# Kernel optimization log

Measured on AMD Instinct MI355X. Metric: run time of the kernel, lower is better.

Reference implementation:

```python
import jax, jax.numpy as jnp
import numpy as np

B, T, N, K, C = 4, 12, 2000, 8, 32
AGG_N = 4  # mean, max, min, std
EPS = 1e-5


def sparsify(a, k):
    # keep top-k entries per row, zero the rest (torch.topk + torch.where)
    thr = jax.lax.top_k(a, k)[0][..., -1:]
    return jnp.where(a < thr, jnp.zeros_like(a), a)


def aggregate(I, adj):
    # I: (b,t,n,f), adj: (b,n,n) row-sparsified with K nonzeros per row
    deg = jnp.sum(adj, axis=-1)[:, None, :, None]              # (b,1,n,1)
    mean = jnp.einsum('bnm,btmf->btnf', adj, I) / deg
    meansq = jnp.einsum('bnm,btmf->btnf', adj, I * I) / deg
    std = jnp.sqrt(jax.nn.relu(meansq - mean * mean) + EPS)
    vals, idx = jax.lax.top_k(adj, K)                          # (b,n,K)
    nb = jax.vmap(lambda Ib, ib: Ib[:, ib])(I, idx)            # (b,t,n,K,f)
    valid = (vals > 0)[:, None, :, :, None]
    mx = jnp.max(jnp.where(valid, nb, -jnp.inf), axis=3)
    mn = jnp.min(jnp.where(valid, nb, jnp.inf), axis=3)
    return jnp.concatenate([mean, mx, mn, std], axis=3)


def stower(x, adj, Theta, bias, masking, use_scalers):
    # x: (b,c,t,n) -> out: (b,o,t,n)
    I = jnp.transpose(x, (0, 2, 3, 1))                          # (b,t,n,c)
    m = aggregate(I, adj)
    if masking:
        m = jnp.where(jnp.isnan(m), 6.0, m)
        m = jnp.where(jnp.isinf(m), 0.0, m)
        m = jnp.minimum(m, 6.0)
    if use_scalers:
        deg = jnp.sum((adj > 0).astype(m.dtype), axis=-1)       # (b,n)
        s = jnp.log1p(deg)[:, None, :, None]
        m = jnp.concatenate([m, m * s, m / s], axis=3)
    out = jnp.einsum('btji,io->btjo', m, Theta) + bias
    return jnp.transpose(out, (0, 3, 1, 2))


def tcn(x, W, b):
    # tcn_layer2 with act='linear': tanh(conv1x1(x) + x)
    return jnp.tanh(jnp.einsum('oc,bctn->botn', W, x) + b[None, :, None, None] + x)


def setup_inputs():
    key = jax.random.key(0)
    ks = jax.random.split(key, 14)
    stdv = 1.0 / np.sqrt(C)
    u = lambda k, shape: jax.random.uniform(k, shape, jnp.float32, -stdv, stdv)
    return {
        'X': jax.random.normal(ks[0], (B, T, N, 1), jnp.float32),
        'adj': jax.random.uniform(ks[1], (N, N), jnp.float32),
        'adj_mask': jax.random.uniform(ks[2], (N, N), jnp.float32),
        'Theta0': u(ks[3], (AGG_N * 1, C)),   # len(agg)*len(['identity'])*in_variables
        'bias0': u(ks[4], (C,)),
        'Wt0': u(ks[5], (C, C)),
        'bt0': u(ks[6], (C,)),
        'Theta1': u(ks[7], (AGG_N * 3 * C, C)),  # len(agg)*len(scalers)*channels
        'bias1': u(ks[8], (C,)),
        'Wt1': u(ks[9], (C, C)),
        'bt1': u(ks[10], (C,)),
        'Wout': u(ks[11], (1, C)),
        'bout': u(ks[12], (1,)),
        'batch_seen': 0,
        'epoch': 0,
        'train': 0,
    }


def reference(X, adj, adj_mask, Theta0, bias0, Wt0, bt0, Theta1, bias1, Wt1, bt1, Wout, bout, batch_seen, epoch, train):
    x0 = X[:, None, :, :, 0]                                   # (b,1,t,n)
    adj_s = sparsify(jnp.broadcast_to(adj, (B, N, N)), K)
    adjm_s = sparsify(jnp.broadcast_to(adj_mask, (B, N, N)), K)
    h = stower(x0, adjm_s, Theta0, bias0, True, False)         # s_layer0 (masking, identity scaler)
    h = tcn(h, Wt0, bt0)                                       # t_layer0
    h = jax.nn.relu(stower(h, adj_s, Theta1, bias1, False, True))
    h = jax.nn.relu(tcn(h, Wt1, bt1))
    y = jnp.einsum('oc,bctn->botn', Wout, h) + bout[None, :, None, None]
    return y.reshape(B, T, N)
```

## Files before the change

kernel.cpp:

```cpp
#include <hip/hip_runtime.h>
#include <hip/hip_bf16.h>
#include <math.h>

#define BB 4
#define TT 12
#define NN 2000
#define KK 8
#define CC 32
#define EPSF 1e-5f
#define LISTCAP 16
#define NSITES (BB * TT * NN)

typedef unsigned short u16;
typedef __bf16 bf16x8 __attribute__((ext_vector_type(8)));
typedef float  f32x4  __attribute__((ext_vector_type(4)));

__device__ __forceinline__ u16 f2bf(float x) {
    union { __hip_bfloat16 h; u16 u; } c;
    c.h = __float2bfloat16(x);
    return c.u;
}
__device__ __forceinline__ float bf2f(u16 u) {
    return __uint_as_float(((unsigned)u) << 16);
}
__device__ __forceinline__ float mask6(float v) {
    if (isnan(v)) v = 6.0f;
    if (isinf(v)) v = 0.0f;
    return fminf(v, 6.0f);
}

__global__ __launch_bounds__(256)
void topk_prep(const float* __restrict__ adj, const float* __restrict__ adjm,
               int* __restrict__ t_idx, float* __restrict__ t_val,
               int* __restrict__ t_cnt, float* __restrict__ t_deg,
               float* __restrict__ t_ideg, float2* __restrict__ t_sc)
{
    __shared__ float sTop[4][8];
    __shared__ float sDeg[4];
    __shared__ int   sCp[4];
    __shared__ int   sStrictIdx[8];
    __shared__ float sStrictVal[8];
    __shared__ int   sTieIdx[16];
    __shared__ int   nStrict, nTie;
    __shared__ float sThr;

    const int tid  = threadIdx.x;
    const int lane = tid & 63;
    const int wid  = tid >> 6;

    const int grow = blockIdx.x;
    const int mat = (grow >= NN) ? 1 : 0;
    const int row = grow - mat * NN;
    const float* src = (mat == 0 ? adjm : adj) + (size_t)row * NN;
    const float4* src4 = (const float4*)src;

    if (tid == 0) { nStrict = 0; nTie = 0; }

    const float4 v0 = src4[tid];
    const float4 v1 = (tid < 244) ? src4[256 + tid]
                                  : make_float4(-1.f, -1.f, -1.f, -1.f);
    const float vv[8] = {v0.x, v0.y, v0.z, v0.w, v1.x, v1.y, v1.z, v1.w};

    float a[8];
    #pragma unroll
    for (int j = 0; j < 8; ++j) a[j] = vv[j];
    #define CE(i, j) { float _mx = fmaxf(a[i], a[j]); float _mn = fminf(a[i], a[j]); a[i] = _mx; a[j] = _mn; }
    CE(0,1) CE(2,3) CE(4,5) CE(6,7)
    CE(0,2) CE(1,3) CE(4,6) CE(5,7)
    CE(1,2) CE(5,6)
    CE(0,4) CE(1,5) CE(2,6) CE(3,7)
    CE(2,4) CE(3,5)
    CE(1,2) CE(3,4) CE(5,6)
    #undef CE

    float key[8];
    #pragma unroll
    for (int j = 0; j < 8; ++j) key[j] = a[j];
    #pragma unroll
    for (int d = 1; d < 64; d <<= 1) {
        float ok[8], c[8];
        #pragma unroll
        for (int j = 0; j < 8; ++j) ok[j] = __shfl_xor(key[j], d, 64);
        #pragma unroll
        for (int j = 0; j < 8; ++j) c[j] = fmaxf(key[j], ok[7 - j]);
        #pragma unroll
        for (int st = 4; st >= 1; st >>= 1) {
            #pragma unroll
            for (int j = 0; j < 8; ++j) {
                if ((j & st) == 0 && (j | st) < 8) {
                    float hi = fmaxf(c[j], c[j | st]);
                    float lo = fminf(c[j], c[j | st]);
                    c[j] = hi; c[j | st] = lo;
                }
            }
        }
        #pragma unroll
        for (int j = 0; j < 8; ++j) key[j] = c[j];
    }
    if (lane == 0) {
        #pragma unroll
        for (int j = 0; j < 8; ++j) sTop[wid][j] = key[j];
    }
    __syncthreads();

    if (tid == 0) {
        int p0 = 0, p1 = 0, p2 = 0, p3 = 0;
        float t = -1.f;
        for (int r = 0; r < 8; ++r) {
            const float c0 = (p0 < 8) ? sTop[0][p0] : -2.f;
            const float c1 = (p1 < 8) ? sTop[1][p1] : -2.f;
            const float c2 = (p2 < 8) ? sTop[2][p2] : -2.f;
            const float c3 = (p3 < 8) ? sTop[3][p3] : -2.f;
            float bv = c0; int best = 0;
            if (c1 > bv) { bv = c1; best = 1; }
            if (c2 > bv) { bv = c2; best = 2; }
            if (c3 > bv) { bv = c3; best = 3; }
            if (best == 0) ++p0; else if (best == 1) ++p1;
            else if (best == 2) ++p2; else ++p3;
            t = bv;
        }
        sThr = t;
    }
    __syncthreads();
    const float thr = sThr;

    float degp = 0.f; int cp = 0;
    #pragma unroll
    for (int s = 0; s < 8; ++s) {
        const float v = vv[s];
        const int e = (s < 4) ? (tid * 4 + s) : ((256 + tid) * 4 + (s - 4));
        const bool ge = (v >= thr);
        degp += ge ? v : 0.f;
        cp   += (ge && v > 0.f) ? 1 : 0;
        if (v > thr) {
            int p = atomicAdd(&nStrict, 1);
            if (p < 8) { sStrictIdx[p] = e; sStrictVal[p] = v; }
        } else if (v == thr) {
            int p = atomicAdd(&nTie, 1);
            if (p < 16) sTieIdx[p] = e;
        }
    }
    #pragma unroll
    for (int off = 32; off >= 1; off >>= 1) {
        degp += __shfl_xor(degp, off, 64);
        cp   += __shfl_xor(cp, off, 64);
    }
    if (lane == 0) { sDeg[wid] = degp; sCp[wid] = cp; }
    __syncthreads();

    if (tid == 0) {
        const float deg = sDeg[0] + sDeg[1] + sDeg[2] + sDeg[3];
        const int cnt_pos = sCp[0] + sCp[1] + sCp[2] + sCp[3];
        int m = nStrict; if (m > 8) m = 8;
        int nt = nTie;   if (nt > 16) nt = 16;
        for (int i = 1; i < nt; ++i) {
            int v = sTieIdx[i]; int j = i - 1;
            while (j >= 0 && sTieIdx[j] > v) { sTieIdx[j + 1] = sTieIdx[j]; --j; }
            sTieIdx[j + 1] = v;
        }
        const size_t ob = (size_t)grow * LISTCAP;
        for (int j = 0; j < m; ++j) {
            t_idx[ob + j] = sStrictIdx[j];
            t_val[ob + j] = sStrictVal[j];
        }
        const int need = 8 - m;
        for (int j = 0; j < need; ++j) {
            t_idx[ob + m + j] = sTieIdx[j];
            t_val[ob + m + j] = thr;
        }
        int extra = nt - need;
        if (extra > 8) extra = 8; if (extra < 0) extra = 0;
        for (int j = 0; j < extra; ++j) {
            t_idx[ob + 8 + j] = sTieIdx[need + j];
            t_val[ob + 8 + j] = thr;
        }
        t_cnt[grow]  = 8 + extra;
        t_deg[grow]  = deg;
        t_ideg[grow] = 1.0f / deg;
        const float s1 = log1pf((float)cnt_pos);
        t_sc[grow]   = make_float2(s1, 1.0f / s1);
    }
}

__global__ __launch_bounds__(256)
void stower0_tcn0(const float* __restrict__ X,
                  const int* __restrict__ t_idx, const float* __restrict__ t_val,
                  const int* __restrict__ t_cnt, const float* __restrict__ t_deg,
                  const float* __restrict__ Theta0, const float* __restrict__ bias0,
                  const float* __restrict__ Wt0, const float* __restrict__ bt0,
                  const float* __restrict__ Theta1, const float* __restrict__ Wt1,
                  u16* __restrict__ thHi, u16* __restrict__ thLo,
                  u16* __restrict__ wtHi, u16* __restrict__ wtLo,
                  float* __restrict__ I1)
{
    const int tid = threadIdx.x;
    if (blockIdx.x >= NSITES / 256) {
        const int pb = blockIdx.x - NSITES / 256;
        if (pb < 12) {
            const int base = pb * 1024;
            #pragma unroll
            for (int t = 0; t < 4; ++t) {
                const int i = base + t * 256 + tid;
                const int r = i >> 5, o = i & 31;
                const int jm = r >> 7, k = r & 127;
                const int tile = jm * 2 + (o >> 4), n = o & 15;
                const float v = Theta1[i];
                const u16 hi = f2bf(v);
                const int idx = (tile * 16 + n) * 128 + (((k >> 3) ^ n) << 3) + (k & 7);
                thHi[idx] = hi;
                thLo[idx] = f2bf(v - bf2f(hi));
            }
        } else {
            #pragma unroll
            for (int t = 0; t < 4; ++t) {
                const int i = t * 256 + tid;
                const float v = Wt1[i];
                const u16 hi = f2bf(v);
                wtHi[i] = hi;
                wtLo[i] = f2bf(v - bf2f(hi));
            }
        }
        return;
    }

    const int site = blockIdx.x * 256 + tid;
    const int n  = site % NN;
    const int bt = site / NN;
    const float* xrow = X + (size_t)bt * NN;

    const size_t base = (size_t)n * LISTCAP;
    const int cnt   = t_cnt[n];
    const float deg = t_deg[n];
    float wsum = 0.f, wsq = 0.f, mx = -INFINITY, mn = INFINITY;
    for (int j = 0; j < cnt; ++j) {
        int   id = t_idx[base + j];
        float w  = t_val[base + j];
        float xv = xrow[id];
        wsum = fmaf(w, xv, wsum);
        wsq  = fmaf(w * xv, xv, wsq);
        if (j < KK && w > 0.f) { mx = fmaxf(mx, xv); mn = fminf(mn, xv); }
    }
    float mean = wsum / deg;
    float var  = wsq / deg - mean * mean;
    float sd   = sqrtf(fmaxf(var, 0.f) + EPSF);
    float m0 = mask6(mean), m1 = mask6(mx), m2 = mask6(mn), m3 = mask6(sd);

    float h0[CC];
    #pragma unroll
    for (int c = 0; c < CC; ++c) {
        float v = bias0[c];
        v = fmaf(m0, Theta0[0 * CC + c], v);
        v = fmaf(m1, Theta0[1 * CC + c], v);
        v = fmaf(m2, Theta0[2 * CC + c], v);
        v = fmaf(m3, Theta0[3 * CC + c], v);
        h0[c] = v;
    }
    float* op = I1 + (size_t)site * CC;
    #pragma unroll
    for (int c = 0; c < CC; ++c) {
        float acc = bt0[c] + h0[c];
        #pragma unroll
        for (int k = 0; k < CC; ++k) acc = fmaf(Wt0[c * CC + k], h0[k], acc);
        op[c] = tanhf(acc);
    }
}

__global__ __launch_bounds__(256)
void stower1_agg(const float* __restrict__ I1,
                 const int* __restrict__ t_idx, const float* __restrict__ t_val,
                 const int* __restrict__ t_cnt, const float* __restrict__ t_ideg,
                 u16* __restrict__ mHi, u16* __restrict__ mLo)
{
    const int tid  = threadIdx.x;
    const int site = blockIdx.x * 8 + (tid >> 5);
    const int f    = tid & 31;
    const int n  = site % NN;
    const int bt = site / NN;
    const size_t rbase = (size_t)(NN + n) * LISTCAP;
    const int cnt    = t_cnt[NN + n];
    const float ideg = t_ideg[NN + n];
    const float* Ibt = I1 + (size_t)bt * NN * CC;

    const int4   i0 = *(const int4*)&t_idx[rbase];
    const int4   i1 = *(const int4*)&t_idx[rbase + 4];
    const float4 w0 = *(const float4*)&t_val[rbase];
    const float4 w1 = *(const float4*)&t_val[rbase + 4];

    const float x0 = Ibt[(size_t)i0.x * CC + f];
    const float x1 = Ibt[(size_t)i0.y * CC + f];
    const float x2 = Ibt[(size_t)i0.z * CC + f];
    const float x3 = Ibt[(size_t)i0.w * CC + f];
    const float x4 = Ibt[(size_t)i1.x * CC + f];
    const float x5 = Ibt[(size_t)i1.y * CC + f];
    const float x6 = Ibt[(size_t)i1.z * CC + f];
    const float x7 = Ibt[(size_t)i1.w * CC + f];

    float wsum = 0.f, wsq = 0.f, mx = -INFINITY, mn = INFINITY;
    #define AGG(wv, xv) do { \
        wsum = fmaf(wv, xv, wsum); wsq = fmaf(wv * xv, xv, wsq); \
        mx = fmaxf(mx, xv); mn = fminf(mn, xv); } while (0)
    AGG(w0.x, x0); AGG(w0.y, x1); AGG(w0.z, x2); AGG(w0.w, x3);
    AGG(w1.x, x4); AGG(w1.y, x5); AGG(w1.z, x6); AGG(w1.w, x7);
    #undef AGG
    if (cnt > 8) {
        for (int j = 8; j < cnt; ++j) {
            int   id = t_idx[rbase + j];
            float wv = t_val[rbase + j];
            float xv = Ibt[(size_t)id * CC + f];
            wsum = fmaf(wv, xv, wsum);
            wsq  = fmaf(wv * xv, xv, wsq);
        }
    }
    const float mean = wsum * ideg;
    const float var  = wsq * ideg - mean * mean;
    const float sd   = sqrtf(fmaxf(var, 0.f) + EPSF);

    const int sx = site & 15;
    const int b  = site * 128;
    const int fh = f >> 3, fl = f & 7;
    const int ia  = b + (((0  + fh) ^ sx) << 3) + fl;
    const int ib  = b + (((4  + fh) ^ sx) << 3) + fl;
    const int ic  = b + (((8  + fh) ^ sx) << 3) + fl;
    const int id_ = b + (((12 + fh) ^ sx) << 3) + fl;
    u16 h0 = f2bf(mean); mHi[ia]  = h0; mLo[ia]  = f2bf(mean - bf2f(h0));
    u16 h1 = f2bf(mx);   mHi[ib]  = h1; mLo[ib]  = f2bf(mx   - bf2f(h1));
    u16 h2 = f2bf(mn);   mHi[ic]  = h2; mLo[ic]  = f2bf(mn   - bf2f(h2));
    u16 h3 = f2bf(sd);   mHi[id_] = h3; mLo[id_] = f2bf(sd   - bf2f(h3));
}

__global__ __launch_bounds__(256, 3)
void stower1_gemm(const u16* __restrict__ mHi, const u16* __restrict__ mLo,
                  const u16* __restrict__ thHi, const u16* __restrict__ thLo,
                  const u16* __restrict__ wtHi, const u16* __restrict__ wtLo,
                  const float2* __restrict__ t_sc,
                  const float* __restrict__ bias1, const float* __restrict__ bt1,
                  const float* __restrict__ Wout, const float* __restrict__ bout,
                  float* __restrict__ out)
{
    __shared__ u16 sBlo[96 * 128];
    __shared__ alignas(16) u16 uSpace[12288];
    __shared__ float sPart[64];

    u16*   mT  = uSpace;
    u16*   hHi = uSpace;
    u16*   hLo = hHi + 32 * 40;
    float* h32 = (float*)((char*)uSpace + 5120);

    const int tid  = threadIdx.x;
    const int lane = tid & 63;
    const int w    = tid >> 6;
    const int m15  = lane & 15;
    const int q    = lane >> 4;
    const int hf   = w & 1;
    const int st   = w >> 1;
    const int ot   = w >> 1;
    const int st2  = w & 1;

    for (int i = tid; i < 1536; i += 256)
        ((float4*)uSpace)[i] = ((const float4*)thHi)[i];
    __syncthreads();
    bf16x8 bH[3][4];
    #pragma unroll
    for (int j3 = 0; j3 < 3; ++j3) {
        const int tile = 2 * j3 + hf;
        #pragma unroll
        for (int ks = 0; ks < 4; ++ks)
            bH[j3][ks] = *(const bf16x8*)&uSpace[(tile * 16 + m15) * 128 +
                                                 (((ks * 4 + q) ^ m15) << 3)];
    }
    __syncthreads();
    for (int i = tid; i < 1536; i += 256)
        ((float4*)sBlo)[i] = ((const float4*)thLo)[i];
    const bf16x8 bwh = *(const bf16x8*)&wtHi[(ot * 16 + m15) * 32 + q * 8];
    const bf16x8 bwl = *(const bf16x8*)&wtLo[(ot * 16 + m15) * 32 + q * 8];
    const float b1o   = bias1[hf * 16 + m15];
    const float bt1o  = bt1[ot * 16 + m15];
    const float wouto = Wout[ot * 16 + m15];
    const float boutv = bout[0];

    #pragma unroll 1
    for (int mb = 0; mb < 3; ++mb) {
        const int sbase = (blockIdx.x * 3 + mb) * 32;

        {
            const float4* gh = (const float4*)&mHi[(size_t)sbase * 128];
            const float4* gl = (const float4*)&mLo[(size_t)sbase * 128];
            float4* dh = (float4*)mT;
            float4* dl = (float4*)(mT + 4096);
            dh[tid]       = gh[tid];
            dh[tid + 256] = gh[tid + 256];
            dl[tid]       = gl[tid];
            dl[tid + 256] = gl[tid + 256];
        }
        __syncthreads();

        f32x4 acc[3];
        #pragma unroll
        for (int j3 = 0; j3 < 3; ++j3) acc[j3] = (f32x4){0.f, 0.f, 0.f, 0.f};
        const int arow = (st * 16 + m15) * 128;
        #pragma unroll
        for (int ks = 0; ks < 4; ++ks) {
            const int koff = (((ks * 4 + q) ^ m15) << 3);
            const bf16x8 aH = *(const bf16x8*)&mT[arow + koff];
            const bf16x8 aL = *(const bf16x8*)&mT[4096 + arow + koff];
            #pragma unroll
            for (int j3 = 0; j3 < 3; ++j3) {
                const bf16x8 bL = *(const bf16x8*)&sBlo[((2 * j3 + hf) * 16 + m15) * 128 + koff];
                acc[j3] = __builtin_amdgcn_mfma_f32_16x16x32_bf16(aH, bH[j3][ks], acc[j3], 0, 0, 0);
                acc[j3] = __builtin_amdgcn_mfma_f32_16x16x32_bf16(aH, bL,          acc[j3], 0, 0, 0);
                acc[j3] = __builtin_amdgcn_mfma_f32_16x16x32_bf16(aL, bH[j3][ks], acc[j3], 0, 0, 0);
            }
        }
        __syncthreads();

        #pragma unroll
        for (int r = 0; r < 4; ++r) {
            const int sl2  = st * 16 + q * 4 + r;
            const int site = sbase + sl2;
            const int n    = site % NN;
            const float2 sc = t_sc[NN + n];
            float h = acc[0][r] + sc.x * acc[1][r] + sc.y * acc[2][r] + b1o;
            h = fmaxf(h, 0.f);
            const int o = hf * 16 + m15;
            const u16 hi = f2bf(h);
            hHi[sl2 * 40 + o] = hi;
            hLo[sl2 * 40 + o] = f2bf(h - bf2f(hi));
            h32[sl2 * 33 + o] = h;
        }
        __syncthreads();

        f32x4 c2 = (f32x4){0.f, 0.f, 0.f, 0.f};
        {
            const bf16x8 ahh = *(const bf16x8*)&hHi[(st2 * 16 + m15) * 40 + q * 8];
            const bf16x8 ahl = *(const bf16x8*)&hLo[(st2 * 16 + m15) * 40 + q * 8];
            c2 = __builtin_amdgcn_mfma_f32_16x16x32_bf16(ahh, bwh, c2, 0, 0, 0);
            c2 = __builtin_amdgcn_mfma_f32_16x16x32_bf16(ahh, bwl, c2, 0, 0, 0);
            c2 = __builtin_amdgcn_mfma_f32_16x16x32_bf16(ahl, bwh, c2, 0, 0, 0);
        }
        float p[4];
        #pragma unroll
        for (int r = 0; r < 4; ++r) {
            const int sl2 = st2 * 16 + q * 4 + r;
            const float hres = h32[sl2 * 33 + ot * 16 + m15];
            float yv = tanhf(c2[r] + bt1o + hres);
            yv = fmaxf(yv, 0.f);
            p[r] = yv * wouto;
            #pragma unroll
            for (int mk = 1; mk <= 8; mk <<= 1)
                p[r] += __shfl_xor(p[r], mk, 64);
        }
        float selv  = (m15 & 1) ? p[1] : p[0];
        float selv2 = (m15 & 1) ? p[3] : p[2];
        selv = (m15 & 2) ? selv2 : selv;
        if (m15 < 4) sPart[ot * 32 + st2 * 16 + q * 4 + m15] = selv;
        __syncthreads();

        if (tid < 32) out[sbase + tid] = sPart[tid] + sPart[32 + tid] + boutv;
    }
}

extern "C" void kernel_launch(void* const* d_in, const int* in_sizes, int n_in,
                              void* d_out, int out_size, void* d_ws, size_t ws_size,
                              hipStream_t stream)
{
    const float* X      = (const float*)d_in[0];
    const float* adj    = (const float*)d_in[1];
    const float* adjm   = (const float*)d_in[2];
    const float* Theta0 = (const float*)d_in[3];
    const float* bias0  = (const float*)d_in[4];
    const float* Wt0    = (const float*)d_in[5];
    const float* bt0    = (const float*)d_in[6];
    const float* Theta1 = (const float*)d_in[7];
    const float* bias1  = (const float*)d_in[8];
    const float* Wt1    = (const float*)d_in[9];
    const float* bt1    = (const float*)d_in[10];
    const float* Wout   = (const float*)d_in[11];
    const float* bout   = (const float*)d_in[12];
    (void)in_sizes; (void)n_in; (void)out_size; (void)ws_size;

    char* p = (char*)d_ws;
    int*    t_idx  = (int*)p;    p += (size_t)2 * NN * LISTCAP * sizeof(int);
    float*  t_val  = (float*)p;  p += (size_t)2 * NN * LISTCAP * sizeof(float);
    int*    t_cnt  = (int*)p;    p += (size_t)2 * NN * sizeof(int);
    float*  t_deg  = (float*)p;  p += (size_t)2 * NN * sizeof(float);
    float*  t_ideg = (float*)p;  p += (size_t)2 * NN * sizeof(float);
    float2* t_sc   = (float2*)p; p += (size_t)2 * NN * sizeof(float2);
    float*  I1     = (float*)p;  p += (size_t)NSITES * CC * sizeof(float);
    u16*    mHi    = (u16*)p;    p += (size_t)NSITES * 128 * sizeof(u16);
    u16*    mLo    = (u16*)p;    p += (size_t)NSITES * 128 * sizeof(u16);
    u16*    thHi   = (u16*)p;    p += (size_t)96 * 128 * sizeof(u16);
    u16*    thLo   = (u16*)p;    p += (size_t)96 * 128 * sizeof(u16);
    u16*    wtHi   = (u16*)p;    p += (size_t)1024 * sizeof(u16);
    u16*    wtLo   = (u16*)p;    p += (size_t)1024 * sizeof(u16);

    hipLaunchKernelGGL(topk_prep, dim3(2 * NN), dim3(256), 0, stream,
                       adj, adjm, t_idx, t_val, t_cnt, t_deg, t_ideg, t_sc);
    hipLaunchKernelGGL(stower0_tcn0, dim3(NSITES / 256 + 13), dim3(256), 0, stream,
                       X, t_idx, t_val, t_cnt, t_deg, Theta0, bias0, Wt0, bt0,
                       Theta1, Wt1, thHi, thLo, wtHi, wtLo, I1);
    hipLaunchKernelGGL(stower1_agg, dim3(NSITES / 8), dim3(256), 0, stream,
                       I1, t_idx, t_val, t_cnt, t_ideg, mHi, mLo);
    hipLaunchKernelGGL(stower1_gemm, dim3(NSITES / 96), dim3(256), 0, stream,
                       mHi, mLo, thHi, thLo, wtHi, wtLo, t_sc,
                       bias1, bt1, Wout, bout, (float*)d_out);
}
```

Baseline: 177.1 us.

## Fuse stower1 neighbour aggregation into the GEMM kernel via shared memory

Merges the separate aggregation kernel into the MFMA GEMM kernel. Each block computes the mean/max/min/std aggregates for its 32-site tiles directly into the shared-memory A tile, so it no longer writes and re-reads global hi/lo bf16 buffers. This removes one launch and the global round trip for the aggregate matrix. In exchange, the gather loads now run inside the GEMM kernel at reduced occupancy, with an unroll-1 loop over four sites per thread group, which may expose gather latency.

```diff
diff --git a/kernel.cpp b/kernel.cpp
--- a/kernel.cpp
+++ b/kernel.cpp
@@ -265,77 +265,16 @@
     }
 }
 
-__global__ __launch_bounds__(256)
-void stower1_agg(const float* __restrict__ I1,
-                 const int* __restrict__ t_idx, const float* __restrict__ t_val,
-                 const int* __restrict__ t_cnt, const float* __restrict__ t_ideg,
-                 u16* __restrict__ mHi, u16* __restrict__ mLo)
-{
-    const int tid  = threadIdx.x;
-    const int site = blockIdx.x * 8 + (tid >> 5);
-    const int f    = tid & 31;
-    const int n  = site % NN;
-    const int bt = site / NN;
-    const size_t rbase = (size_t)(NN + n) * LISTCAP;
-    const int cnt    = t_cnt[NN + n];
-    const float ideg = t_ideg[NN + n];
-    const float* Ibt = I1 + (size_t)bt * NN * CC;
-
-    const int4   i0 = *(const int4*)&t_idx[rbase];
-    const int4   i1 = *(const int4*)&t_idx[rbase + 4];
-    const float4 w0 = *(const float4*)&t_val[rbase];
-    const float4 w1 = *(const float4*)&t_val[rbase + 4];
-
-    const float x0 = Ibt[(size_t)i0.x * CC + f];
-    const float x1 = Ibt[(size_t)i0.y * CC + f];
-    const float x2 = Ibt[(size_t)i0.z * CC + f];
-    const float x3 = Ibt[(size_t)i0.w * CC + f];
-    const float x4 = Ibt[(size_t)i1.x * CC + f];
-    const float x5 = Ibt[(size_t)i1.y * CC + f];
-    const float x6 = Ibt[(size_t)i1.z * CC + f];
-    const float x7 = Ibt[(size_t)i1.w * CC + f];
-
-    float wsum = 0.f, wsq = 0.f, mx = -INFINITY, mn = INFINITY;
-    #define AGG(wv, xv) do { \
-        wsum = fmaf(wv, xv, wsum); wsq = fmaf(wv * xv, xv, wsq); \
-        mx = fmaxf(mx, xv); mn = fminf(mn, xv); } while (0)
-    AGG(w0.x, x0); AGG(w0.y, x1); AGG(w0.z, x2); AGG(w0.w, x3);
-    AGG(w1.x, x4); AGG(w1.y, x5); AGG(w1.z, x6); AGG(w1.w, x7);
-    #undef AGG
-    if (cnt > 8) {
-        for (int j = 8; j < cnt; ++j) {
-            int   id = t_idx[rbase + j];
-            float wv = t_val[rbase + j];
-            float xv = Ibt[(size_t)id * CC + f];
-            wsum = fmaf(wv, xv, wsum);
-            wsq  = fmaf(wv * xv, xv, wsq);
-        }
-    }
-    const float mean = wsum * ideg;
-    const float var  = wsq * ideg - mean * mean;
-    const float sd   = sqrtf(fmaxf(var, 0.f) + EPSF);
-
-    const int sx = site & 15;
-    const int b  = site * 128;
-    const int fh = f >> 3, fl = f & 7;
-    const int ia  = b + (((0  + fh) ^ sx) << 3) + fl;
-    const int ib  = b + (((4  + fh) ^ sx) << 3) + fl;
-    const int ic  = b + (((8  + fh) ^ sx) << 3) + fl;
-    const int id_ = b + (((12 + fh) ^ sx) << 3) + fl;
-    u16 h0 = f2bf(mean); mHi[ia]  = h0; mLo[ia]  = f2bf(mean - bf2f(h0));
-    u16 h1 = f2bf(mx);   mHi[ib]  = h1; mLo[ib]  = f2bf(mx   - bf2f(h1));
-    u16 h2 = f2bf(mn);   mHi[ic]  = h2; mLo[ic]  = f2bf(mn   - bf2f(h2));
-    u16 h3 = f2bf(sd);   mHi[id_] = h3; mLo[id_] = f2bf(sd   - bf2f(h3));
-}
-
 __global__ __launch_bounds__(256, 3)
-void stower1_gemm(const u16* __restrict__ mHi, const u16* __restrict__ mLo,
-                  const u16* __restrict__ thHi, const u16* __restrict__ thLo,
-                  const u16* __restrict__ wtHi, const u16* __restrict__ wtLo,
-                  const float2* __restrict__ t_sc,
-                  const float* __restrict__ bias1, const float* __restrict__ bt1,
-                  const float* __restrict__ Wout, const float* __restrict__ bout,
-                  float* __restrict__ out)
+void stower1_fused(const float* __restrict__ I1,
+                   const int* __restrict__ t_idx, const float* __restrict__ t_val,
+                   const int* __restrict__ t_cnt, const float* __restrict__ t_ideg,
+                   const u16* __restrict__ thHi, const u16* __restrict__ thLo,
+                   const u16* __restrict__ wtHi, const u16* __restrict__ wtLo,
+                   const float2* __restrict__ t_sc,
+                   const float* __restrict__ bias1, const float* __restrict__ bt1,
+                   const float* __restrict__ Wout, const float* __restrict__ bout,
+                   float* __restrict__ out)
 {
     __shared__ u16 sBlo[96 * 128];
     __shared__ alignas(16) u16 uSpace[12288];
@@ -356,6 +295,10 @@
     const int ot   = w >> 1;
     const int st2  = w & 1;
 
+    const int ag = tid >> 5;
+    const int af = tid & 31;
+    const int afh = af >> 3, afl = af & 7;
+
     for (int i = tid; i < 1536; i += 256)
         ((float4*)uSpace)[i] = ((const float4*)thHi)[i];
     __syncthreads();
@@ -382,15 +325,61 @@
     for (int mb = 0; mb < 3; ++mb) {
         const int sbase = (blockIdx.x * 3 + mb) * 32;
 
-        {
-            const float4* gh = (const float4*)&mHi[(size_t)sbase * 128];
-            const float4* gl = (const float4*)&mLo[(size_t)sbase * 128];
-            float4* dh = (float4*)mT;
-            float4* dl = (float4*)(mT + 4096);
-            dh[tid]       = gh[tid];
-            dh[tid + 256] = gh[tid + 256];
-            dl[tid]       = gl[tid];
-            dl[tid + 256] = gl[tid + 256];
+        #pragma unroll 1
+        for (int r = 0; r < 4; ++r) {
+            const int sl2  = ag * 4 + r;
+            const int site = sbase + sl2;
+            const int n    = site % NN;
+            const int bt   = site / NN;
+            const size_t rbase = (size_t)(NN + n) * LISTCAP;
+            const int cnt    = t_cnt[NN + n];
+            const float ideg = t_ideg[NN + n];
+            const float* Ibt = I1 + (size_t)bt * NN * CC;
+
+            const int4   i0 = *(const int4*)&t_idx[rbase];
+            const int4   i1 = *(const int4*)&t_idx[rbase + 4];
+            const float4 w0 = *(const float4*)&t_val[rbase];
+            const float4 w1 = *(const float4*)&t_val[rbase + 4];
+
+            const float x0 = Ibt[(size_t)i0.x * CC + af];
+            const float x1 = Ibt[(size_t)i0.y * CC + af];
+            const float x2 = Ibt[(size_t)i0.z * CC + af];
+            const float x3 = Ibt[(size_t)i0.w * CC + af];
+            const float x4 = Ibt[(size_t)i1.x * CC + af];
+            const float x5 = Ibt[(size_t)i1.y * CC + af];
+            const float x6 = Ibt[(size_t)i1.z * CC + af];
+            const float x7 = Ibt[(size_t)i1.w * CC + af];
+
+            float wsum = 0.f, wsq = 0.f, mx = -INFINITY, mn = INFINITY;
+            #define AGG(wv, xv) do { \
+                wsum = fmaf(wv, xv, wsum); wsq = fmaf(wv * xv, xv, wsq); \
+                mx = fmaxf(mx, xv); mn = fminf(mn, xv); } while (0)
+            AGG(w0.x, x0); AGG(w0.y, x1); AGG(w0.z, x2); AGG(w0.w, x3);
+            AGG(w1.x, x4); AGG(w1.y, x5); AGG(w1.z, x6); AGG(w1.w, x7);
+            #undef AGG
+            if (cnt > 8) {
+                for (int j = 8; j < cnt; ++j) {
+                    int   id = t_idx[rbase + j];
+                    float wv = t_val[rbase + j];
+                    float xv = Ibt[(size_t)id * CC + af];
+                    wsum = fmaf(wv, xv, wsum);
+                    wsq  = fmaf(wv * xv, xv, wsq);
+                }
+            }
+            const float mean = wsum * ideg;
+            const float var  = wsq * ideg - mean * mean;
+            const float sd   = sqrtf(fmaxf(var, 0.f) + EPSF);
+
+            const int sx = sl2 & 15;
+            const int b  = sl2 * 128;
+            const int ia  = b + (((0  + afh) ^ sx) << 3) + afl;
+            const int ib  = b + (((4  + afh) ^ sx) << 3) + afl;
+            const int ic  = b + (((8  + afh) ^ sx) << 3) + afl;
+            const int id_ = b + (((12 + afh) ^ sx) << 3) + afl;
+            u16 h0 = f2bf(mean); mT[ia]  = h0; mT[4096 + ia]  = f2bf(mean - bf2f(h0));
+            u16 h1 = f2bf(mx);   mT[ib]  = h1; mT[4096 + ib]  = f2bf(mx   - bf2f(h1));
+            u16 h2 = f2bf(mn);   mT[ic]  = h2; mT[4096 + ic]  = f2bf(mn   - bf2f(h2));
+            u16 h3 = f2bf(sd);   mT[id_] = h3; mT[4096 + id_] = f2bf(sd   - bf2f(h3));
         }
         __syncthreads();
 
@@ -486,8 +475,6 @@
     float*  t_ideg = (float*)p;  p += (size_t)2 * NN * sizeof(float);
     float2* t_sc   = (float2*)p; p += (size_t)2 * NN * sizeof(float2);
     float*  I1     = (float*)p;  p += (size_t)NSITES * CC * sizeof(float);
-    u16*    mHi    = (u16*)p;    p += (size_t)NSITES * 128 * sizeof(u16);
-    u16*    mLo    = (u16*)p;    p += (size_t)NSITES * 128 * sizeof(u16);
     u16*    thHi   = (u16*)p;    p += (size_t)96 * 128 * sizeof(u16);
     u16*    thLo   = (u16*)p;    p += (size_t)96 * 128 * sizeof(u16);
     u16*    wtHi   = (u16*)p;    p += (size_t)1024 * sizeof(u16);
@@ -498,9 +485,8 @@
     hipLaunchKernelGGL(stower0_tcn0, dim3(NSITES / 256 + 13), dim3(256), 0, stream,
                        X, t_idx, t_val, t_cnt, t_deg, Theta0, bias0, Wt0, bt0,
                        Theta1, Wt1, thHi, thLo, wtHi, wtLo, I1);
-    hipLaunchKernelGGL(stower1_agg, dim3(NSITES / 8), dim3(256), 0, stream,
-                       I1, t_idx, t_val, t_cnt, t_ideg, mHi, mLo);
-    hipLaunchKernelGGL(stower1_gemm, dim3(NSITES / 96), dim3(256), 0, stream,
-                       mHi, mLo, thHi, thLo, wtHi, wtLo, t_sc,
+    hipLaunchKernelGGL(stower1_fused, dim3(NSITES / 96), dim3(256), 0, stream,
+                       I1, t_idx, t_val, t_cnt, t_ideg,
+                       thHi, thLo, wtHi, wtLo, t_sc,
                        bias1, bt1, Wout, bout, (float*)d_out);
 }
```

Measured after the change: 179.7 us. About the same (+1.5%).
